# Kernel tuning notes

Hardware: AMD Instinct MI355X
Metric: run time of the kernel (lower is better)

Reference implementation:

```python
import jax, jax.numpy as jnp
import numpy as np

H = 256; NH = 8; DH = H // NH; L = 2; B = 32; S = 512; FIN = 199; A = 4


def _ln(x, g, b):
    m = jnp.mean(x, -1, keepdims=True)
    v = jnp.mean((x - m) ** 2, -1, keepdims=True)
    return (x - m) / jnp.sqrt(v + 1e-5) * g + b


def _grn(x, fc1w, fc1b, fc2w, fc2b, gw, gb, ggw, ggb, lg, lb):
    # GatedResidualNetwork, input_dim == output_dim so no skip layer, no context
    h = jax.nn.elu(x @ fc1w + fc1b)
    h = jax.nn.elu(h @ fc2w + fc2b)
    g = (h @ gw + gb) * jax.nn.sigmoid(h @ ggw + ggb)  # GLU
    return _ln(g + x, lg, lb)


def _attn(h, wq, bq, wk, bk, wv, bv, wo, bo):
    b, s, _ = h.shape
    q = (h @ wq + bq).reshape(b, s, NH, DH)
    k = (h @ wk + bk).reshape(b, s, NH, DH)
    v = (h @ wv + bv).reshape(b, s, NH, DH)
    scores = jnp.einsum('bqhd,bkhd->bhqk', q, k) / jnp.sqrt(jnp.float32(DH))
    mask = jnp.triu(jnp.ones((s, s), dtype=bool), 1)  # causal: mask strictly-future
    scores = jnp.where(mask, -jnp.inf, scores)
    aw = jax.nn.softmax(scores, axis=-1)
    ctx = jnp.einsum('bhqk,bkhd->bqhd', aw, v).reshape(b, s, H)
    return ctx @ wo + bo, aw


def _pe(s, d):
    pos = jnp.arange(s, dtype=jnp.float32)[:, None]
    div = jnp.exp(jnp.arange(0, d, 2, dtype=jnp.float32) * (-jnp.log(10000.0) / d))
    pe = jnp.zeros((s, d), dtype=jnp.float32)
    pe = pe.at[:, 0::2].set(jnp.sin(pos * div)).at[:, 1::2].set(jnp.cos(pos * div))
    return pe


def setup_inputs():
    key = jax.random.key(0)
    ks = iter(jax.random.split(key, 80))
    def nrm(shape, sc=0.02):
        return (jax.random.normal(next(ks), shape) * sc).astype(jnp.float32)
    d = {}
    d['x'] = jax.random.normal(next(ks), (B, S, FIN), dtype=jnp.float32)
    d['time_features'] = jax.random.normal(next(ks), (B, S, 3), dtype=jnp.float32)
    d['fp_w'] = nrm((FIN, H)); d['fp_b'] = jnp.zeros((H,), jnp.float32)
    d['tp_w'] = nrm((3, H));   d['tp_b'] = jnp.zeros((H,), jnp.float32)
    d['ip_w'] = nrm((H, H));   d['ip_b'] = jnp.zeros((H,), jnp.float32)
    for nm in ['wq', 'wk', 'wv', 'wo']:
        d[nm] = nrm((L, H, H))
    for nm in ['bq', 'bk', 'bv', 'bo']:
        d[nm] = jnp.zeros((L, H), jnp.float32)
    d['ln_g'] = jnp.ones((L, H), jnp.float32); d['ln_b'] = jnp.zeros((L, H), jnp.float32)
    for nm in ['g_fc1w', 'g_fc2w', 'g_gw', 'g_ggw']:
        d[nm] = nrm((L, H, H))
    for nm in ['g_fc1b', 'g_fc2b', 'g_gb', 'g_ggb']:
        d[nm] = jnp.zeros((L, H), jnp.float32)
    d['g_lg'] = jnp.ones((L, H), jnp.float32); d['g_lb'] = jnp.zeros((L, H), jnp.float32)
    for nm in ['f_fc1w', 'f_fc2w', 'f_gw', 'f_ggw']:
        d[nm] = nrm((H, H))
    for nm in ['f_fc1b', 'f_fc2b', 'f_gb', 'f_ggb']:
        d[nm] = jnp.zeros((H,), jnp.float32)
    d['f_lg'] = jnp.ones((H,), jnp.float32); d['f_lb'] = jnp.zeros((H,), jnp.float32)
    d['out_w'] = nrm((H, A)); d['out_b'] = jnp.zeros((A,), jnp.float32)
    return d


def reference(x, time_features, fp_w, fp_b, tp_w, tp_b, ip_w, ip_b,
              wq, bq, wk, bk, wv, bv, wo, bo, ln_g, ln_b,
              g_fc1w, g_fc1b, g_fc2w, g_fc2b, g_gw, g_gb, g_ggw, g_ggb, g_lg, g_lb,
              f_fc1w, f_fc1b, f_fc2w, f_fc2b, f_gw, f_gb, f_ggw, f_ggb, f_lg, f_lb,
              out_w, out_b):
    s = x.shape[1]
    hidden = (x @ fp_w + fp_b) + (time_features @ tp_w + tp_b)
    hidden = hidden @ ip_w + ip_b
    hidden = hidden + _pe(s, H)[None]
    aw = None
    for i in range(L):
        ao, aw = _attn(hidden, wq[i], bq[i], wk[i], bk[i], wv[i], bv[i], wo[i], bo[i])
        hidden = _ln(hidden + ao, ln_g[i], ln_b[i])
        hidden = _grn(hidden, g_fc1w[i], g_fc1b[i], g_fc2w[i], g_fc2b[i],
                      g_gw[i], g_gb[i], g_ggw[i], g_ggb[i], g_lg[i], g_lb[i])
    hidden = _grn(hidden, f_fc1w, f_fc1b, f_fc2w, f_fc2b, f_gw, f_gb, f_ggw, f_ggb, f_lg, f_lb)
    final = hidden[:, -1, :]
    logits = final @ out_w + out_b  # [B, A], one column per target asset
    return (logits, aw)
```

## Files before the change

### kernel.cpp

```cpp
#include <hip/hip_runtime.h>
#include <hip/hip_fp16.h>
#include <math.h>
#include <cstddef>

#define H 256
#define NH 8
#define DH 32
#define LAYERS 2
#define BB 32
#define SS 512
#define FINDIM 199
#define AA 4
#define T_TOK (BB*SS)
#define KIN 224
#define TPB 64

typedef unsigned short u16;
typedef unsigned int u32;
typedef __attribute__((ext_vector_type(8))) short short8;
typedef __attribute__((ext_vector_type(4))) float f4;

__device__ __forceinline__ float b2f(u16 v){
  unsigned u = ((unsigned)v) << 16;
  return __builtin_bit_cast(float, u);
}
__device__ __forceinline__ u16 f2b(float f){
  unsigned u = __builtin_bit_cast(unsigned, f);
  unsigned r = (u + 0x7fffu + ((u >> 16) & 1u)) >> 16;
  return (u16)r;
}
__device__ __forceinline__ float wave_sum(float v){
  #pragma unroll
  for (int mk=1; mk<64; mk<<=1) v += __shfl_xor(v, mk, 64);
  return v;
}

#define GLD_LDS16(g, l) \
  __builtin_amdgcn_global_load_lds((const __attribute__((address_space(1))) void*)(g), \
                                   (__attribute__((address_space(3))) void*)(l), 16, 0, 0)

#define SA (KIN+8)
#define SY (H+8)

template<int KC, int WK>
__device__ __forceinline__ void stage_acc64(
    const u16* Xl, int sx, const u16* __restrict__ Wt,
    int r0, int c0, int l16, int lq, f4 acc[2][4])
{
  #pragma unroll
  for (int mi=0;mi<2;mi++)
    #pragma unroll
    for (int ni=0;ni<4;ni++) acc[mi][ni] = (f4){0.f,0.f,0.f,0.f};
  #pragma unroll
  for (int kc=0;kc<KC;kc++){
    short8 af[2], bf[4];
    #pragma unroll
    for (int mi=0;mi<2;mi++)
      af[mi] = *(const short8*)&Xl[(r0 + mi*16 + l16)*sx + kc*32 + lq*8];
    #pragma unroll
    for (int ni=0;ni<4;ni++)
      bf[ni] = *(const short8*)(Wt + (size_t)(c0 + ni*16 + l16)*WK + kc*32 + lq*8);
    #pragma unroll
    for (int mi=0;mi<2;mi++)
      #pragma unroll
      for (int ni=0;ni<4;ni++)
        acc[mi][ni] = __builtin_amdgcn_mfma_f32_16x16x32_bf16(af[mi], bf[ni], acc[mi][ni], 0,0,0);
  }
}

template<int DO_ELU>
__device__ __forceinline__ void stage_store64(
    f4 acc[2][4], const float* __restrict__ bias,
    int r0, int c0, int l16, int lq, u16* Yl, int sy)
{
  #pragma unroll
  for (int ni=0;ni<4;ni++){
    int col = c0 + ni*16 + l16;
    float bc = bias[col];
    #pragma unroll
    for (int mi=0;mi<2;mi++){
      #pragma unroll
      for (int r=0;r<4;r++){
        int row = r0 + mi*16 + lq*4 + r;
        float v = acc[mi][ni][r] + bc;
        if (DO_ELU) v = v > 0.f ? v : expm1f(v);
        Yl[row*sy + col] = f2b(v);
      }
    }
  }
}

__device__ __forceinline__ void tile_load64(const u16* g, u16* Yl, int sy, int t){
  #pragma unroll
  for (int j=0;j<4;j++){
    int u = t + j*512;
    int row = u >> 5, cu = u & 31;
    *(short8*)&Yl[row*sy + cu*8] = *(const short8*)(g + (size_t)row*H + cu*8);
  }
}

template<int WB>
__device__ __forceinline__ void tile_ln64(
    u16* Yl, int sy, const float* __restrict__ g, const float* __restrict__ b,
    u16* out, int t)
{
  int w = t >> 6, lane = t & 63;
  #pragma unroll
  for (int rr=0;rr<8;rr++){
    int row = w*8 + rr;
    float xv[4];
    #pragma unroll
    for (int j=0;j<4;j++) xv[j] = b2f(Yl[row*sy + lane*4 + j]);
    float s=0.f, ss=0.f;
    #pragma unroll
    for (int j=0;j<4;j++){ s += xv[j]; ss += xv[j]*xv[j]; }
    s = wave_sum(s); ss = wave_sum(ss);
    float mean = s * (1.0f/H);
    float var  = ss * (1.0f/H) - mean*mean;
    float rstd = rsqrtf(var + 1e-5f);
    ushort4 o;
    int col = lane*4;
    o.x = f2b((xv[0]-mean)*rstd*g[col+0] + b[col+0]);
    o.y = f2b((xv[1]-mean)*rstd*g[col+1] + b[col+1]);
    o.z = f2b((xv[2]-mean)*rstd*g[col+2] + b[col+2]);
    o.w = f2b((xv[3]-mean)*rstd*g[col+3] + b[col+3]);
    *(ushort4*)(out + (size_t)row*H + col) = o;
    if (WB && row == 63) *(ushort4*)(Yl + row*sy + col) = o;
  }
}

struct WPtrs { const float* p[21]; };

__global__ __launch_bounds__(256) void wconv_kernel(WPtrs wp, u16* __restrict__ dst){
  __shared__ float tl[64][65];
  int mb = blockIdx.x >> 4, tile = blockIdx.x & 15;
  int k0 = (tile >> 2) * 64, n0 = (tile & 3) * 64;
  const float* src = wp.p[mb];
  int t = threadIdx.x;
  int r = t >> 4, cg = t & 15;
  #pragma unroll
  for (int p4=0;p4<4;p4++){
    f4 v = *(const f4*)(src + (size_t)(k0 + r + p4*16)*H + n0 + cg*4);
    tl[r+p4*16][cg*4+0]=v[0]; tl[r+p4*16][cg*4+1]=v[1];
    tl[r+p4*16][cg*4+2]=v[2]; tl[r+p4*16][cg*4+3]=v[3];
  }
  __syncthreads();
  u16* db = dst + (size_t)mb*H*H;
  #pragma unroll
  for (int p4=0;p4<4;p4++){
    int rn = r + p4*16;
    ushort4 o;
    o.x = f2b(tl[cg*4+0][rn]); o.y = f2b(tl[cg*4+1][rn]);
    o.z = f2b(tl[cg*4+2][rn]); o.w = f2b(tl[cg*4+3][rn]);
    *(ushort4*)(db + (size_t)(n0+rn)*H + k0 + cg*4) = o;
  }
}

__global__ __launch_bounds__(256) void wcat_kernel(
    const float* __restrict__ fp_w, const float* __restrict__ tp_w,
    u16* __restrict__ wcat){
  int idx = blockIdx.x*256 + threadIdx.x;
  if (idx >= 256*KIN) return;
  int n = idx / KIN, k2 = idx % KIN;
  float v = 0.f;
  if (k2 < FINDIM) v = fp_w[(size_t)k2*H + n];
  else if (k2 < FINDIM+3) v = tp_w[(size_t)(k2-FINDIM)*H + n];
  wcat[idx] = f2b(v);
}

__global__ __launch_bounds__(256) void xconv_kernel(
    const float* __restrict__ x, const float* __restrict__ tf,
    u16* __restrict__ ab){
  size_t idx = (size_t)blockIdx.x*256 + threadIdx.x;
  if (idx >= (size_t)T_TOK*KIN) return;
  int tok = idx / KIN, k2 = idx % KIN;
  float v = 0.f;
  if (k2 < FINDIM) v = x[(size_t)tok*FINDIM + k2];
  else if (k2 < FINDIM+3) v = tf[(size_t)tok*3 + (k2-FINDIM)];
  ab[idx] = f2b(v);
}

__global__ __launch_bounds__(512,2) void input_kernel(
    const u16* __restrict__ ab, const u16* __restrict__ wcat,
    const float* __restrict__ fp_b, const float* __restrict__ tp_b,
    const u16* __restrict__ ipw, const float* __restrict__ ip_b,
    u16* __restrict__ hid){
  __shared__ u16 Al[TPB*SA];
  __shared__ u16 Tl[TPB*SY];
  int t = threadIdx.x;
  int tok0 = blockIdx.x * TPB;
  int lane = t & 63, w = t >> 6;
  int l16 = lane & 15, lq = lane >> 4;
  int r0 = (w >> 2) * 32;
  int c0 = (w & 3) * 64;

  #pragma unroll
  for (int j=0;j<4;j++){
    int u = t + j*512;
    if (u < 1792){
      int row = u / 28, cu = u % 28;
      *(short8*)&Al[row*SA + cu*8] = *(const short8*)(ab + (size_t)(tok0+row)*KIN + cu*8);
    }
  }
  __syncthreads();

  f4 acc[2][4];
  stage_acc64<7, KIN>(Al, SA, wcat, r0, c0, l16, lq, acc);
  #pragma unroll
  for (int ni=0;ni<4;ni++){
    int col = c0 + ni*16 + l16;
    float bc = fp_b[col] + tp_b[col];
    #pragma unroll
    for (int mi=0;mi<2;mi++)
      #pragma unroll
      for (int r=0;r<4;r++){
        int row = r0 + mi*16 + lq*4 + r;
        Tl[row*SY + col] = f2b(acc[mi][ni][r] + bc);
      }
  }
  __syncthreads();

  stage_acc64<8, H>(Tl, SY, ipw, r0, c0, l16, lq, acc);
  #pragma unroll
  for (int ni=0;ni<4;ni++){
    int col = c0 + ni*16 + l16;
    float bc = ip_b[col];
    int ii = col >> 1;
    float div = __expf((float)(2*ii) * -0.03597789207803197f);
    #pragma unroll
    for (int mi=0;mi<2;mi++)
      #pragma unroll
      for (int r=0;r<4;r++){
        int row = r0 + mi*16 + lq*4 + r;
        int s = (tok0 + row) & (SS-1);
        float arg = (float)s * div;
        float pe = (col & 1) ? cosf(arg) : sinf(arg);
        hid[(size_t)(tok0+row)*H + col] = f2b(acc[mi][ni][r] + bc + pe);
      }
  }
}

__global__ __launch_bounds__(512,2) void oproj_ln_kernel(
    const u16* __restrict__ ctx, u16* __restrict__ hid,
    const u16* __restrict__ wo, const float* __restrict__ bo,
    const float* __restrict__ g, const float* __restrict__ b){
  __shared__ u16 Xl[TPB*SY];
  __shared__ u16 Rl[TPB*SY];
  int t = threadIdx.x;
  int tok0 = blockIdx.x * TPB;
  int lane = t & 63, w = t >> 6;
  int l16 = lane & 15, lq = lane >> 4;
  int r0 = (w >> 2) * 32;
  int c0 = (w & 3) * 64;
  u16* hb = hid + (size_t)tok0*H;

  tile_load64(ctx + (size_t)tok0*H, Xl, SY, t);
  tile_load64(hb, Rl, SY, t);
  __syncthreads();

  f4 acc[2][4];
  stage_acc64<8, H>(Xl, SY, wo, r0, c0, l16, lq, acc);
  __syncthreads();
  #pragma unroll
  for (int ni=0;ni<4;ni++){
    int col = c0 + ni*16 + l16;
    float bc = bo[col];
    #pragma unroll
    for (int mi=0;mi<2;mi++)
      #pragma unroll
      for (int r=0;r<4;r++){
        int row = r0 + mi*16 + lq*4 + r;
        float y = acc[mi][ni][r] + bc + b2f(Rl[row*SY + col]);
        Xl[row*SY + col] = f2b(y);
      }
  }
  __syncthreads();
  tile_ln64<0>(Xl, SY, g, b, hb, t);
}

template<int LOGITS>
__global__ __launch_bounds__(512,2) void grn_kernel(
    u16* __restrict__ hid,
    const u16* __restrict__ fc1, const u16* __restrict__ fc2,
    const u16* __restrict__ gw,  const u16* __restrict__ ggw,
    const float* __restrict__ b1, const float* __restrict__ b2,
    const float* __restrict__ gb, const float* __restrict__ ggb,
    const float* __restrict__ lg, const float* __restrict__ lb,
    const float* __restrict__ ow, const float* __restrict__ ob,
    float* __restrict__ lout){
  __shared__ u16 Xa[TPB*SY];
  __shared__ u16 Xb[TPB*SY];
  int t = threadIdx.x;
  int tok0 = blockIdx.x * TPB;
  int lane = t & 63, w = t >> 6;
  int l16 = lane & 15, lq = lane >> 4;
  int r0 = (w >> 2) * 32;
  int c0 = (w & 3) * 64;
  u16* hb = hid + (size_t)tok0*H;

  tile_load64(hb, Xa, SY, t);
  __syncthreads();

  f4 acc[2][4];
  stage_acc64<8, H>(Xa, SY, fc1, r0, c0, l16, lq, acc);
  stage_store64<1>(acc, b1, r0, c0, l16, lq, Xb, SY);
  __syncthreads();
  stage_acc64<8, H>(Xb, SY, fc2, r0, c0, l16, lq, acc);
  __syncthreads();
  stage_store64<1>(acc, b2, r0, c0, l16, lq, Xb, SY);
  __syncthreads();

  stage_acc64<8, H>(Xb, SY, ggw, r0, c0, l16, lq, acc);
  u32 sgp[2][4][2];
  #pragma unroll
  for (int mi=0;mi<2;mi++)
    #pragma unroll
    for (int ni=0;ni<4;ni++){
      float bc = ggb[c0 + ni*16 + l16];
      float s0 = 1.0f/(1.0f + __expf(-(acc[mi][ni][0]+bc)));
      float s1 = 1.0f/(1.0f + __expf(-(acc[mi][ni][1]+bc)));
      float s2 = 1.0f/(1.0f + __expf(-(acc[mi][ni][2]+bc)));
      float s3 = 1.0f/(1.0f + __expf(-(acc[mi][ni][3]+bc)));
      sgp[mi][ni][0] = __builtin_bit_cast(u32, __floats2half2_rn(s0, s1));
      sgp[mi][ni][1] = __builtin_bit_cast(u32, __floats2half2_rn(s2, s3));
    }

  stage_acc64<8, H>(Xb, SY, gw, r0, c0, l16, lq, acc);
  __syncthreads();
  #pragma unroll
  for (int ni=0;ni<4;ni++){
    int col = c0 + ni*16 + l16;
    float bc = gb[col];
    #pragma unroll
    for (int mi=0;mi<2;mi++){
      float2 s01 = __half22float2(__builtin_bit_cast(__half2, sgp[mi][ni][0]));
      float2 s23 = __half22float2(__builtin_bit_cast(__half2, sgp[mi][ni][1]));
      float sv[4] = {s01.x, s01.y, s23.x, s23.y};
      #pragma unroll
      for (int r=0;r<4;r++){
        int row = r0 + mi*16 + lq*4 + r;
        float y = (acc[mi][ni][r] + bc) * sv[r] + b2f(Xa[row*SY + col]);
        Xb[row*SY + col] = f2b(y);
      }
    }
  }
  __syncthreads();
  tile_ln64<LOGITS>(Xb, SY, lg, lb, hb, t);

  if (LOGITS){
    if ((tok0 & (SS-1)) == SS - TPB){
      __syncthreads();
      if (t < 64){
        int bidx = tok0 >> 9;
        float a0=0.f, a1=0.f, a2=0.f, a3=0.f;
        #pragma unroll
        for (int j=0;j<4;j++){
          int k = t*4 + j;
          float xv = b2f(Xb[63*SY + k]);
          f4 wr = *(const f4*)(ow + (size_t)k*AA);
          a0 = fmaf(xv, wr[0], a0);
          a1 = fmaf(xv, wr[1], a1);
          a2 = fmaf(xv, wr[2], a2);
          a3 = fmaf(xv, wr[3], a3);
        }
        a0 = wave_sum(a0); a1 = wave_sum(a1);
        a2 = wave_sum(a2); a3 = wave_sum(a3);
        if (t == 0){
          lout[bidx*AA+0] = a0 + ob[0];
          lout[bidx*AA+1] = a1 + ob[1];
          lout[bidx*AA+2] = a2 + ob[2];
          lout[bidx*AA+3] = a3 + ob[3];
        }
      }
    }
  }
}

struct GemmJob  { const u16* Wt; const float* bias; u16* C; };
struct GemmBatch{ GemmJob j[3]; };

__global__ __launch_bounds__(256) void gemm_bf16(
    const u16* __restrict__ A, GemmBatch jb) {
  __shared__ u16 smem[128*64 + 64*64];
  u16* As  = smem;
  u16* Wsm = smem + 128*64;
  const GemmJob job = jb.j[blockIdx.z];
  const u16* Wt = job.Wt;
  int t = threadIdx.x;
  int m0 = blockIdx.x * 128;
  int n0 = blockIdx.y * 64;
  int lane = t & 63, w = t >> 6;
  int wr = (w >> 1) * 64;
  int wc = (w & 1) * 32;
  int l16 = lane & 15, lq = lane >> 4;

  f4 acc[4][2];
  #pragma unroll
  for (int mi=0;mi<4;mi++)
    #pragma unroll
    for (int ni=0;ni<2;ni++) acc[mi][ni] = (f4){0.f,0.f,0.f,0.f};

  for (int k0=0;k0<256;k0+=64){
    #pragma unroll
    for (int ja=0;ja<4;ja++){
      int ub = (w*4 + ja)*64;
      int u  = ub + lane;
      int m  = u >> 3, c = u & 7, kx = c ^ (m & 7);
      const u16* g = A + (size_t)(m0+m)*H + k0 + kx*8;
      GLD_LDS16(g, As + (size_t)ub*8);
    }
    #pragma unroll
    for (int jb2=0;jb2<2;jb2++){
      int ub = (w*2 + jb2)*64;
      int u  = ub + lane;
      int n  = u >> 3, c = u & 7, kx = c ^ (n & 7);
      const u16* g = Wt + (size_t)(n0+n)*H + k0 + kx*8;
      GLD_LDS16(g, Wsm + (size_t)ub*8);
    }
    __syncthreads();
    #pragma unroll
    for (int kc=0;kc<2;kc++){
      short8 af[4], bf[2];
      int kx = kc*4 + lq;
      #pragma unroll
      for (int mi=0;mi<4;mi++){
        int m = wr + mi*16 + l16;
        int un = (m<<3) | (kx ^ (m&7));
        af[mi] = *(short8*)&As[un*8];
      }
      #pragma unroll
      for (int ni=0;ni<2;ni++){
        int n = wc + ni*16 + l16;
        int un = (n<<3) | (kx ^ (n&7));
        bf[ni] = *(short8*)&Wsm[un*8];
      }
      #pragma unroll
      for (int mi=0;mi<4;mi++)
        #pragma unroll
        for (int ni=0;ni<2;ni++)
          acc[mi][ni] = __builtin_amdgcn_mfma_f32_16x16x32_bf16(af[mi], bf[ni], acc[mi][ni], 0,0,0);
    }
    __syncthreads();
  }

  u16* Cl = smem;
  #pragma unroll
  for (int ni=0;ni<2;ni++){
    int coll = wc + ni*16 + l16;
    float bcol = job.bias[n0 + coll];
    #pragma unroll
    for (int mi=0;mi<4;mi++){
      #pragma unroll
      for (int r=0;r<4;r++){
        int rowl = wr + mi*16 + lq*4 + r;
        Cl[rowl*68 + coll] = f2b(acc[mi][ni][r] + bcol);
      }
    }
  }
  __syncthreads();
  #pragma unroll
  for (int q2=0;q2<4;q2++){
    int u = q2*256 + t;
    int row = u >> 3, cu = u & 7;
    short8 val = *(short8*)&Cl[row*68 + cu*8];
    *(short8*)(job.C + (size_t)(m0+row)*H + n0 + cu*8) = val;
  }
}

template<int WRITE_AW>
__global__ __launch_bounds__(512) void attn_kernel(
    const u16* __restrict__ q, const u16* __restrict__ k,
    const u16* __restrict__ v, float* __restrict__ aw,
    u16* __restrict__ ctx) {
  __shared__ u16 Vt[DH][SS+8];
  __shared__ u16 Plds[8][16][72];
  int t  = threadIdx.x;
  int zg = blockIdx.x;
  int bh = blockIdx.y;
  int b  = bh >> 3, h = bh & 7;
  int lane = t & 63, w = t >> 6;
  int l16 = lane & 15, lq = lane >> 4;
  const float scale = 0.17677669529663687f;

  int nrows = (zg+1)*128;
  for (int kk = t; kk < nrows; kk += 512){
    const u16* vp = v + ((size_t)(b*SS + kk))*H + h*DH;
    short8 r0v = *(const short8*)(vp);
    short8 r1v = *(const short8*)(vp+8);
    short8 r2v = *(const short8*)(vp+16);
    short8 r3v = *(const short8*)(vp+24);
    #pragma unroll
    for (int j=0;j<8;j++){
      Vt[j][kk]    = (u16)r0v[j];
      Vt[8+j][kk]  = (u16)r1v[j];
      Vt[16+j][kk] = (u16)r2v[j];
      Vt[24+j][kk] = (u16)r3v[j];
    }
  }
  __syncthreads();

  {
    int qt  = zg*2 + (w >> 2);
    int wq  = w & 3;
    int qr0 = qt*64 + wq*16;
    int KT  = qt*4 + wq + 1;
    short8 af = *(const short8*)(q + ((size_t)(b*SS + qr0 + l16))*H + h*DH + lq*8);

    float l[4] = {0.f,0.f,0.f,0.f};
    f4 o[2] = {(f4){0.f,0.f,0.f,0.f}, (f4){0.f,0.f,0.f,0.f}};

    #pragma unroll
    for (int c8=0;c8<8;c8++){
      if (c8*4 < KT){
        #pragma unroll
        for (int j=0;j<4;j++){
          int kt = c8*4 + j;
          float p[4] = {0.f,0.f,0.f,0.f};
          if (kt < KT){
            short8 bfr = *(const short8*)(k + ((size_t)(b*SS + kt*16 + l16))*H + h*DH + lq*8);
            f4 cc = (f4){0.f,0.f,0.f,0.f};
            cc = __builtin_amdgcn_mfma_f32_16x16x32_bf16(af, bfr, cc, 0,0,0);
            int col = kt*16 + l16;
            #pragma unroll
            for (int i=0;i<4;i++){
              int qi = qr0 + lq*4 + i;
              float sc = (col <= qi) ? cc[i]*scale : -3.0e38f;
              p[i] = __expf(sc);
              l[i] += p[i];
            }
          }
          #pragma unroll
          for (int i=0;i<4;i++) Plds[w][lq*4+i][j*16+l16] = f2b(p[i]);
        }
        #pragma unroll
        for (int kc=0;kc<2;kc++){
          short8 pa = *(short8*)&Plds[w][l16][kc*32 + lq*8];
          #pragma unroll
          for (int dt=0;dt<2;dt++){
            short8 vb = *(const short8*)&Vt[dt*16 + l16][c8*64 + kc*32 + lq*8];
            o[dt] = __builtin_amdgcn_mfma_f32_16x16x32_bf16(pa, vb, o[dt], 0,0,0);
          }
        }
      }
    }

    #pragma unroll
    for (int i=0;i<4;i++){
      #pragma unroll
      for (int mk=1; mk<16; mk<<=1) l[i] += __shfl_xor(l[i], mk, 64);
    }
    float inv[4];
    #pragma unroll
    for (int i=0;i<4;i++) inv[i] = 1.0f / l[i];

    if (WRITE_AW){
      float* ab = aw + (size_t)bh*SS*SS;
      for (int kt=0; kt<KT; kt++){
        short8 bfr = *(const short8*)(k + ((size_t)(b*SS + kt*16 + l16))*H + h*DH + lq*8);
        f4 cc = (f4){0.f,0.f,0.f,0.f};
        cc = __builtin_amdgcn_mfma_f32_16x16x32_bf16(af, bfr, cc, 0,0,0);
        int col = kt*16 + l16;
        #pragma unroll
        for (int i=0;i<4;i++){
          int qi = qr0 + lq*4 + i;
          float val = (col <= qi) ? __expf(cc[i]*scale)*inv[i] : 0.f;
          __builtin_nontemporal_store(val, &ab[(size_t)qi*SS + col]);
        }
      }
      int c4base = KT*4;
      f4 z = (f4){0.f,0.f,0.f,0.f};
      #pragma unroll
      for (int ri=0;ri<4;ri++){
        int row = qr0 + ri*4 + lq;
        for (int j=l16; j < 128 - c4base; j += 16)
          __builtin_nontemporal_store(z, (f4*)&ab[(size_t)row*SS + (size_t)(c4base+j)*4]);
      }
    }

    #pragma unroll
    for (int dt=0;dt<2;dt++){
      #pragma unroll
      for (int i=0;i<4;i++){
        int row = qr0 + lq*4 + i;
        ctx[((size_t)(b*SS + row))*H + h*DH + dt*16 + l16] = f2b(o[dt][i]*inv[i]);
      }
    }
  }
}

extern "C" void kernel_launch(void* const* d_in, const int* in_sizes, int n_in,
                              void* d_out, int out_size, void* d_ws, size_t ws_size,
                              hipStream_t stream){
  (void)in_sizes; (void)n_in; (void)out_size; (void)ws_size;
  const float* x      = (const float*)d_in[0];
  const float* tf     = (const float*)d_in[1];
  const float* fp_w   = (const float*)d_in[2];
  const float* fp_b   = (const float*)d_in[3];
  const float* tp_w   = (const float*)d_in[4];
  const float* tp_b   = (const float*)d_in[5];
  const float* ip_w   = (const float*)d_in[6];
  const float* ip_b   = (const float*)d_in[7];
  const float* wq     = (const float*)d_in[8];
  const float* wk     = (const float*)d_in[9];
  const float* wv     = (const float*)d_in[10];
  const float* wo     = (const float*)d_in[11];
  const float* bq     = (const float*)d_in[12];
  const float* bk     = (const float*)d_in[13];
  const float* bv     = (const float*)d_in[14];
  const float* bo     = (const float*)d_in[15];
  const float* ln_g   = (const float*)d_in[16];
  const float* ln_b   = (const float*)d_in[17];
  const float* g_fc1w = (const float*)d_in[18];
  const float* g_fc2w = (const float*)d_in[19];
  const float* g_gw   = (const float*)d_in[20];
  const float* g_ggw  = (const float*)d_in[21];
  const float* g_fc1b = (const float*)d_in[22];
  const float* g_fc2b = (const float*)d_in[23];
  const float* g_gb   = (const float*)d_in[24];
  const float* g_ggb  = (const float*)d_in[25];
  const float* g_lg   = (const float*)d_in[26];
  const float* g_lb   = (const float*)d_in[27];
  const float* f_fc1w = (const float*)d_in[28];
  const float* f_fc2w = (const float*)d_in[29];
  const float* f_gw   = (const float*)d_in[30];
  const float* f_ggw  = (const float*)d_in[31];
  const float* f_fc1b = (const float*)d_in[32];
  const float* f_fc2b = (const float*)d_in[33];
  const float* f_gb   = (const float*)d_in[34];
  const float* f_ggb  = (const float*)d_in[35];
  const float* f_lg   = (const float*)d_in[36];
  const float* f_lb   = (const float*)d_in[37];
  const float* out_w  = (const float*)d_in[38];
  const float* out_b  = (const float*)d_in[39];

  float* logits = (float*)d_out;
  float* aw     = logits + BB*AA;

  u16* wts = (u16*)d_ws;
  const size_t WMAT = (size_t)H*H;
  u16* wcat = wts  + 21*WMAT;
  u16* abuf = wcat + (size_t)H*KIN;
  u16* hid  = abuf + (size_t)T_TOK*KIN;
  size_t BUF = (size_t)T_TOK * H;
  u16* buf1 = hid  + BUF;
  u16* buf2 = buf1 + BUF;
  u16* buf3 = buf2 + BUF;

  WPtrs wp;
  wp.p[0]  = ip_w;
  wp.p[1]  = wq;        wp.p[2]  = wq + WMAT;
  wp.p[3]  = wk;        wp.p[4]  = wk + WMAT;
  wp.p[5]  = wv;        wp.p[6]  = wv + WMAT;
  wp.p[7]  = wo;        wp.p[8]  = wo + WMAT;
  wp.p[9]  = g_fc1w;    wp.p[10] = g_fc1w + WMAT;
  wp.p[11] = g_fc2w;    wp.p[12] = g_fc2w + WMAT;
  wp.p[13] = g_gw;      wp.p[14] = g_gw + WMAT;
  wp.p[15] = g_ggw;     wp.p[16] = g_ggw + WMAT;
  wp.p[17] = f_fc1w;    wp.p[18] = f_fc2w;
  wp.p[19] = f_gw;      wp.p[20] = f_ggw;
  const int WT_IP=0, WT_Q=1, WT_K=3, WT_V=5, WT_O=7,
            WT_FC1=9, WT_FC2=11, WT_GW=13, WT_GGW=15,
            WT_FFC1=17, WT_FFC2=18, WT_FGW=19, WT_FGGW=20;

  dim3 b256(256), b512(512);
  dim3 gAttn(4, BB*NH);
  dim3 gTok(T_TOK/TPB);

  wconv_kernel<<<21*16, b256, 0, stream>>>(wp, wts);
  wcat_kernel<<<(H*KIN+255)/256, b256, 0, stream>>>(fp_w, tp_w, wcat);
  xconv_kernel<<<(T_TOK*KIN+255)/256, b256, 0, stream>>>(x, tf, abuf);
  input_kernel<<<gTok, b512, 0, stream>>>(abuf, wcat, fp_b, tp_b,
                                          wts + (size_t)WT_IP*WMAT, ip_b, hid);

  for (int i=0;i<LAYERS;i++){
    const size_t BOFF = (size_t)i*H;
    GemmBatch gb;
    gb.j[0] = { wts + (size_t)(WT_Q+i)*WMAT, bq+BOFF, buf1 };
    gb.j[1] = { wts + (size_t)(WT_K+i)*WMAT, bk+BOFF, buf2 };
    gb.j[2] = { wts + (size_t)(WT_V+i)*WMAT, bv+BOFF, buf3 };
    gemm_bf16<<<dim3(T_TOK/128, H/64, 3), b256, 0, stream>>>(hid, gb);
    if (i == LAYERS-1)
      attn_kernel<1><<<gAttn, b512, 0, stream>>>(buf1, buf2, buf3, aw, buf1);
    else
      attn_kernel<0><<<gAttn, b512, 0, stream>>>(buf1, buf2, buf3, aw, buf1);
    oproj_ln_kernel<<<gTok, b512, 0, stream>>>(buf1, hid,
        wts + (size_t)(WT_O+i)*WMAT, bo+BOFF, ln_g+BOFF, ln_b+BOFF);
    grn_kernel<0><<<gTok, b512, 0, stream>>>(hid,
        wts + (size_t)(WT_FC1+i)*WMAT, wts + (size_t)(WT_FC2+i)*WMAT,
        wts + (size_t)(WT_GW+i)*WMAT,  wts + (size_t)(WT_GGW+i)*WMAT,
        g_fc1b+BOFF, g_fc2b+BOFF, g_gb+BOFF, g_ggb+BOFF,
        g_lg+BOFF, g_lb+BOFF, nullptr, nullptr, nullptr);
  }

  grn_kernel<1><<<gTok, b512, 0, stream>>>(hid,
      wts + (size_t)WT_FFC1*WMAT, wts + (size_t)WT_FFC2*WMAT,
      wts + (size_t)WT_FGW*WMAT,  wts + (size_t)WT_FGGW*WMAT,
      f_fc1b, f_fc2b, f_gb, f_ggb, f_lg, f_lb,
      out_w, out_b, logits);
}
```

Measured before the change: 666.0 us.

## Move attention-weight writeout into output-projection kernel as extra blocks

The last layer's attention kernel no longer writes the full causal attention-weight matrix. It stores only the per-row softmax reciprocal sums. Extra blocks appended to the output-projection/LayerNorm launch recompute QK^T and write the normalized weights, plus the zero fill, so this bandwidth-heavy store runs alongside the projection work instead of serializing the attention kernel. Attention output now goes to a separate buffer so Q stays intact for the recompute. The cost is a second QK^T pass and extra workspace.

```diff
diff --git a/kernel.cpp b/kernel.cpp
--- a/kernel.cpp
+++ b/kernel.cpp
@@ -240,16 +240,59 @@
   }
 }
 
+template<int AW>
 __global__ __launch_bounds__(512,2) void oproj_ln_kernel(
     const u16* __restrict__ ctx, u16* __restrict__ hid,
     const u16* __restrict__ wo, const float* __restrict__ bo,
-    const float* __restrict__ g, const float* __restrict__ b){
+    const float* __restrict__ g, const float* __restrict__ b,
+    const u16* __restrict__ q, const u16* __restrict__ k,
+    const float* __restrict__ linv, float* __restrict__ aw){
   __shared__ u16 Xl[TPB*SY];
   __shared__ u16 Rl[TPB*SY];
+  int bid = blockIdx.x;
   int t = threadIdx.x;
-  int tok0 = blockIdx.x * TPB;
   int lane = t & 63, w = t >> 6;
   int l16 = lane & 15, lq = lane >> 4;
+
+  if (AW && bid >= T_TOK/TPB){
+    int bh = bid - T_TOK/TPB;
+    int b2 = bh >> 3, h = bh & 7;
+    const float scale = 0.17677669529663687f;
+    float* ab = aw + (size_t)bh*SS*SS;
+    int qt = w;
+    #pragma unroll
+    for (int s=0;s<4;s++){
+      int qr0 = qt*64 + s*16;
+      int KT  = qt*4 + s + 1;
+      short8 af = *(const short8*)(q + ((size_t)(b2*SS + qr0 + l16))*H + h*DH + lq*8);
+      float iv[4];
+      #pragma unroll
+      for (int i=0;i<4;i++) iv[i] = linv[(size_t)bh*SS + qr0 + lq*4 + i];
+      for (int kt=0; kt<KT; kt++){
+        short8 bfr = *(const short8*)(k + ((size_t)(b2*SS + kt*16 + l16))*H + h*DH + lq*8);
+        f4 cc = (f4){0.f,0.f,0.f,0.f};
+        cc = __builtin_amdgcn_mfma_f32_16x16x32_bf16(af, bfr, cc, 0,0,0);
+        int col = kt*16 + l16;
+        #pragma unroll
+        for (int i=0;i<4;i++){
+          int qi = qr0 + lq*4 + i;
+          float val = (col <= qi) ? __expf(cc[i]*scale)*iv[i] : 0.f;
+          __builtin_nontemporal_store(val, &ab[(size_t)qi*SS + col]);
+        }
+      }
+      int c4base = KT*4;
+      f4 z = (f4){0.f,0.f,0.f,0.f};
+      #pragma unroll
+      for (int ri=0;ri<4;ri++){
+        int row = qr0 + ri*4 + lq;
+        for (int j=l16; j < 128 - c4base; j += 16)
+          __builtin_nontemporal_store(z, (f4*)&ab[(size_t)row*SS + (size_t)(c4base+j)*4]);
+      }
+    }
+    return;
+  }
+
+  int tok0 = bid * TPB;
   int r0 = (w >> 2) * 32;
   int c0 = (w & 3) * 64;
   u16* hb = hid + (size_t)tok0*H;
@@ -467,10 +510,10 @@
   }
 }
 
-template<int WRITE_AW>
+template<int SAVE_L>
 __global__ __launch_bounds__(512) void attn_kernel(
     const u16* __restrict__ q, const u16* __restrict__ k,
-    const u16* __restrict__ v, float* __restrict__ aw,
+    const u16* __restrict__ v, float* __restrict__ linv,
     u16* __restrict__ ctx) {
   __shared__ u16 Vt[DH][SS+8];
   __shared__ u16 Plds[8][16][72];
@@ -553,27 +596,11 @@
     #pragma unroll
     for (int i=0;i<4;i++) inv[i] = 1.0f / l[i];
 
-    if (WRITE_AW){
-      float* ab = aw + (size_t)bh*SS*SS;
-      for (int kt=0; kt<KT; kt++){
-        short8 bfr = *(const short8*)(k + ((size_t)(b*SS + kt*16 + l16))*H + h*DH + lq*8);
-        f4 cc = (f4){0.f,0.f,0.f,0.f};
-        cc = __builtin_amdgcn_mfma_f32_16x16x32_bf16(af, bfr, cc, 0,0,0);
-        int col = kt*16 + l16;
+    if (SAVE_L){
+      if (l16 == 0){
         #pragma unroll
-        for (int i=0;i<4;i++){
-          int qi = qr0 + lq*4 + i;
-          float val = (col <= qi) ? __expf(cc[i]*scale)*inv[i] : 0.f;
-          __builtin_nontemporal_store(val, &ab[(size_t)qi*SS + col]);
-        }
-      }
-      int c4base = KT*4;
-      f4 z = (f4){0.f,0.f,0.f,0.f};
-      #pragma unroll
-      for (int ri=0;ri<4;ri++){
-        int row = qr0 + ri*4 + lq;
-        for (int j=l16; j < 128 - c4base; j += 16)
-          __builtin_nontemporal_store(z, (f4*)&ab[(size_t)row*SS + (size_t)(c4base+j)*4]);
+        for (int i=0;i<4;i++)
+          linv[(size_t)bh*SS + qr0 + lq*4 + i] = inv[i];
       }
     }
 
@@ -645,6 +672,8 @@
   u16* buf1 = hid  + BUF;
   u16* buf2 = buf1 + BUF;
   u16* buf3 = buf2 + BUF;
+  u16* buf4 = buf3 + BUF;
+  float* linv = (float*)(buf4 + BUF);
 
   WPtrs wp;
   wp.p[0]  = ip_w;
@@ -679,12 +708,17 @@
     gb.j[1] = { wts + (size_t)(WT_K+i)*WMAT, bk+BOFF, buf2 };
     gb.j[2] = { wts + (size_t)(WT_V+i)*WMAT, bv+BOFF, buf3 };
     gemm_bf16<<<dim3(T_TOK/128, H/64, 3), b256, 0, stream>>>(hid, gb);
-    if (i == LAYERS-1)
-      attn_kernel<1><<<gAttn, b512, 0, stream>>>(buf1, buf2, buf3, aw, buf1);
-    else
-      attn_kernel<0><<<gAttn, b512, 0, stream>>>(buf1, buf2, buf3, aw, buf1);
-    oproj_ln_kernel<<<gTok, b512, 0, stream>>>(buf1, hid,
-        wts + (size_t)(WT_O+i)*WMAT, bo+BOFF, ln_g+BOFF, ln_b+BOFF);
+    if (i == LAYERS-1){
+      attn_kernel<1><<<gAttn, b512, 0, stream>>>(buf1, buf2, buf3, linv, buf4);
+      oproj_ln_kernel<1><<<dim3(T_TOK/TPB + BB*NH), b512, 0, stream>>>(
+          buf4, hid, wts + (size_t)(WT_O+i)*WMAT, bo+BOFF, ln_g+BOFF, ln_b+BOFF,
+          buf1, buf2, linv, aw);
+    } else {
+      attn_kernel<0><<<gAttn, b512, 0, stream>>>(buf1, buf2, buf3, linv, buf4);
+      oproj_ln_kernel<0><<<gTok, b512, 0, stream>>>(
+          buf4, hid, wts + (size_t)(WT_O+i)*WMAT, bo+BOFF, ln_g+BOFF, ln_b+BOFF,
+          nullptr, nullptr, nullptr, nullptr);
+    }
     grn_kernel<0><<<gTok, b512, 0, stream>>>(hid,
         wts + (size_t)(WT_FC1+i)*WMAT, wts + (size_t)(WT_FC2+i)*WMAT,
         wts + (size_t)(WT_GW+i)*WMAT,  wts + (size_t)(WT_GGW+i)*WMAT,
```

Result: slower. 690.4 us (+3.7%).

## Split attention key range across two wave groups per query tile

Applied to the files above, without the earlier changes.

Each block now handles one 64-row query tile instead of two, and the grid doubles in x. The two groups of four waves each take half of the key chunks for the same query rows, then merge partial row sums and outputs through LDS before normalising. The aw write is split the same way. This is meant to balance the causal work and raise parallelism, at the cost of extra syncs, an LDS reduction, and reloading V per block.

```diff
diff --git a/kernel.cpp b/kernel.cpp
--- a/kernel.cpp
+++ b/kernel.cpp
@@ -475,14 +475,14 @@
   __shared__ u16 Vt[DH][SS+8];
   __shared__ u16 Plds[8][16][72];
   int t  = threadIdx.x;
-  int zg = blockIdx.x;
+  int qt = blockIdx.x;
   int bh = blockIdx.y;
   int b  = bh >> 3, h = bh & 7;
   int lane = t & 63, w = t >> 6;
   int l16 = lane & 15, lq = lane >> 4;
   const float scale = 0.17677669529663687f;
 
-  int nrows = (zg+1)*128;
+  int nrows = (qt+1)*64;
   for (int kk = t; kk < nrows; kk += 512){
     const u16* vp = v + ((size_t)(b*SS + kk))*H + h*DH;
     short8 r0v = *(const short8*)(vp);
@@ -499,63 +499,24 @@
   }
   __syncthreads();
 
-  {
-    int qt  = zg*2 + (w >> 2);
-    int wq  = w & 3;
-    int qr0 = qt*64 + wq*16;
-    int KT  = qt*4 + wq + 1;
-    short8 af = *(const short8*)(q + ((size_t)(b*SS + qr0 + l16))*H + h*DH + lq*8);
-
-    float l[4] = {0.f,0.f,0.f,0.f};
-    f4 o[2] = {(f4){0.f,0.f,0.f,0.f}, (f4){0.f,0.f,0.f,0.f}};
-
-    #pragma unroll
-    for (int c8=0;c8<8;c8++){
-      if (c8*4 < KT){
-        #pragma unroll
-        for (int j=0;j<4;j++){
-          int kt = c8*4 + j;
-          float p[4] = {0.f,0.f,0.f,0.f};
-          if (kt < KT){
-            short8 bfr = *(const short8*)(k + ((size_t)(b*SS + kt*16 + l16))*H + h*DH + lq*8);
-            f4 cc = (f4){0.f,0.f,0.f,0.f};
-            cc = __builtin_amdgcn_mfma_f32_16x16x32_bf16(af, bfr, cc, 0,0,0);
-            int col = kt*16 + l16;
-            #pragma unroll
-            for (int i=0;i<4;i++){
-              int qi = qr0 + lq*4 + i;
-              float sc = (col <= qi) ? cc[i]*scale : -3.0e38f;
-              p[i] = __expf(sc);
-              l[i] += p[i];
-            }
-          }
-          #pragma unroll
-          for (int i=0;i<4;i++) Plds[w][lq*4+i][j*16+l16] = f2b(p[i]);
-        }
-        #pragma unroll
-        for (int kc=0;kc<2;kc++){
-          short8 pa = *(short8*)&Plds[w][l16][kc*32 + lq*8];
-          #pragma unroll
-          for (int dt=0;dt<2;dt++){
-            short8 vb = *(const short8*)&Vt[dt*16 + l16][c8*64 + kc*32 + lq*8];
-            o[dt] = __builtin_amdgcn_mfma_f32_16x16x32_bf16(pa, vb, o[dt], 0,0,0);
-          }
-        }
-      }
-    }
-
-    #pragma unroll
-    for (int i=0;i<4;i++){
-      #pragma unroll
-      for (int mk=1; mk<16; mk<<=1) l[i] += __shfl_xor(l[i], mk, 64);
-    }
-    float inv[4];
-    #pragma unroll
-    for (int i=0;i<4;i++) inv[i] = 1.0f / l[i];
-
-    if (WRITE_AW){
-      float* ab = aw + (size_t)bh*SS*SS;
-      for (int kt=0; kt<KT; kt++){
+  int s   = w & 3;
+  int qr0 = qt*64 + s*16;
+  int KT  = qt*4 + s + 1;
+  int G   = (KT + 3) >> 2;
+  int gh  = (G + 1) >> 1;
+  int g0  = (w < 4) ? 0  : gh;
+  int g1  = (w < 4) ? gh : G;
+  short8 af = *(const short8*)(q + ((size_t)(b*SS + qr0 + l16))*H + h*DH + lq*8);
+
+  float l[4] = {0.f,0.f,0.f,0.f};
+  f4 o[2] = {(f4){0.f,0.f,0.f,0.f}, (f4){0.f,0.f,0.f,0.f}};
+
+  for (int c8 = g0; c8 < g1; c8++){
+    #pragma unroll
+    for (int j=0;j<4;j++){
+      int kt = c8*4 + j;
+      float p[4] = {0.f,0.f,0.f,0.f};
+      if (kt < KT){
         short8 bfr = *(const short8*)(k + ((size_t)(b*SS + kt*16 + l16))*H + h*DH + lq*8);
         f4 cc = (f4){0.f,0.f,0.f,0.f};
         cc = __builtin_amdgcn_mfma_f32_16x16x32_bf16(af, bfr, cc, 0,0,0);
@@ -563,10 +524,89 @@
         #pragma unroll
         for (int i=0;i<4;i++){
           int qi = qr0 + lq*4 + i;
-          float val = (col <= qi) ? __expf(cc[i]*scale)*inv[i] : 0.f;
-          __builtin_nontemporal_store(val, &ab[(size_t)qi*SS + col]);
+          float sc = (col <= qi) ? cc[i]*scale : -3.0e38f;
+          p[i] = __expf(sc);
+          l[i] += p[i];
         }
       }
+      #pragma unroll
+      for (int i=0;i<4;i++) Plds[w][lq*4+i][j*16+l16] = f2b(p[i]);
+    }
+    #pragma unroll
+    for (int kc=0;kc<2;kc++){
+      short8 pa = *(short8*)&Plds[w][l16][kc*32 + lq*8];
+      #pragma unroll
+      for (int dt=0;dt<2;dt++){
+        short8 vb = *(const short8*)&Vt[dt*16 + l16][c8*64 + kc*32 + lq*8];
+        o[dt] = __builtin_amdgcn_mfma_f32_16x16x32_bf16(pa, vb, o[dt], 0,0,0);
+      }
+    }
+  }
+
+  float* Pf = (float*)&Plds[0][0][0];
+  __syncthreads();
+  if (w >= 4){
+    float* dst = Pf + ((size_t)s*64 + lane)*13;
+    #pragma unroll
+    for (int i=0;i<4;i++) dst[i]   = l[i];
+    #pragma unroll
+    for (int i=0;i<4;i++) dst[4+i] = o[0][i];
+    #pragma unroll
+    for (int i=0;i<4;i++) dst[8+i] = o[1][i];
+  }
+  __syncthreads();
+  float inv[4];
+  if (w < 4){
+    float* src = Pf + ((size_t)s*64 + lane)*13;
+    #pragma unroll
+    for (int i=0;i<4;i++) l[i]    += src[i];
+    #pragma unroll
+    for (int i=0;i<4;i++) o[0][i] += src[4+i];
+    #pragma unroll
+    for (int i=0;i<4;i++) o[1][i] += src[8+i];
+    #pragma unroll
+    for (int i=0;i<4;i++){
+      #pragma unroll
+      for (int mk=1; mk<16; mk<<=1) l[i] += __shfl_xor(l[i], mk, 64);
+      inv[i] = 1.0f / l[i];
+    }
+    #pragma unroll
+    for (int dt=0;dt<2;dt++){
+      #pragma unroll
+      for (int i=0;i<4;i++){
+        int row = qr0 + lq*4 + i;
+        ctx[((size_t)(b*SS + row))*H + h*DH + dt*16 + l16] = f2b(o[dt][i]*inv[i]);
+      }
+    }
+    if (WRITE_AW){
+      #pragma unroll
+      for (int i=0;i<4;i++) src[i] = inv[i];
+    }
+  }
+
+  if (WRITE_AW){
+    __syncthreads();
+    if (w >= 4){
+      const float* src = Pf + ((size_t)s*64 + lane)*13;
+      #pragma unroll
+      for (int i=0;i<4;i++) inv[i] = src[i];
+    }
+    float* ab = aw + (size_t)bh*SS*SS;
+    int k_lo = g0*4;
+    int k_hi = (g1*4 < KT) ? g1*4 : KT;
+    for (int kt = k_lo; kt < k_hi; kt++){
+      short8 bfr = *(const short8*)(k + ((size_t)(b*SS + kt*16 + l16))*H + h*DH + lq*8);
+      f4 cc = (f4){0.f,0.f,0.f,0.f};
+      cc = __builtin_amdgcn_mfma_f32_16x16x32_bf16(af, bfr, cc, 0,0,0);
+      int col = kt*16 + l16;
+      #pragma unroll
+      for (int i=0;i<4;i++){
+        int qi = qr0 + lq*4 + i;
+        float val = (col <= qi) ? __expf(cc[i]*scale)*inv[i] : 0.f;
+        __builtin_nontemporal_store(val, &ab[(size_t)qi*SS + col]);
+      }
+    }
+    if (w >= 4){
       int c4base = KT*4;
       f4 z = (f4){0.f,0.f,0.f,0.f};
       #pragma unroll
@@ -574,15 +614,6 @@
         int row = qr0 + ri*4 + lq;
         for (int j=l16; j < 128 - c4base; j += 16)
           __builtin_nontemporal_store(z, (f4*)&ab[(size_t)row*SS + (size_t)(c4base+j)*4]);
-      }
-    }
-
-    #pragma unroll
-    for (int dt=0;dt<2;dt++){
-      #pragma unroll
-      for (int i=0;i<4;i++){
-        int row = qr0 + lq*4 + i;
-        ctx[((size_t)(b*SS + row))*H + h*DH + dt*16 + l16] = f2b(o[dt][i]*inv[i]);
       }
     }
   }
@@ -663,7 +694,7 @@
             WT_FFC1=17, WT_FFC2=18, WT_FGW=19, WT_FGGW=20;
 
   dim3 b256(256), b512(512);
-  dim3 gAttn(4, BB*NH);
+  dim3 gAttn(8, BB*NH);
   dim3 gTok(T_TOK/TPB);
 
   wconv_kernel<<<21*16, b256, 0, stream>>>(wp, wts);
```

Result: no change. 663.2 us (-0.4%).

## Compute transposed scores in attention to keep P in registers, dropping LDS round-trip

Applied to the files above, without the earlier changes.

The attention kernel now computes S^T (K as the A operand, Q as B), so each lane already holds the probabilities in the layout the P·V MFMA wants. P goes straight into packed bf16 operand registers via v_cvt_pk_bf16_f32 instead of being written to a per-wave LDS tile and read back. The V operand is rebuilt from two 32-bit pairs to match the permuted k ordering. This removes LDS stores, reads and the implicit wave sync per chunk, at the cost of scattered 4-byte V loads from LDS and an extra shuffle to redistribute the row normalizers. The ctx store is also moved ahead of the attention-weight writes.

```diff
diff --git a/kernel.cpp b/kernel.cpp
--- a/kernel.cpp
+++ b/kernel.cpp
@@ -19,6 +19,7 @@
 typedef unsigned int u32;
 typedef __attribute__((ext_vector_type(8))) short short8;
 typedef __attribute__((ext_vector_type(4))) float f4;
+typedef __attribute__((ext_vector_type(4))) unsigned int u32x4;
 
 __device__ __forceinline__ float b2f(u16 v){
   unsigned u = ((unsigned)v) << 16;
@@ -28,6 +29,11 @@
   unsigned u = __builtin_bit_cast(unsigned, f);
   unsigned r = (u + 0x7fffu + ((u >> 16) & 1u)) >> 16;
   return (u16)r;
+}
+__device__ __forceinline__ u32 cvt_pk_bf16(float lo, float hi){
+  u32 r;
+  asm volatile("v_cvt_pk_bf16_f32 %0, %1, %2" : "=v"(r) : "v"(lo), "v"(hi));
+  return r;
 }
 __device__ __forceinline__ float wave_sum(float v){
   #pragma unroll
@@ -473,7 +479,6 @@
     const u16* __restrict__ v, float* __restrict__ aw,
     u16* __restrict__ ctx) {
   __shared__ u16 Vt[DH][SS+8];
-  __shared__ u16 Plds[8][16][72];
   int t  = threadIdx.x;
   int zg = blockIdx.x;
   int bh = blockIdx.y;
@@ -506,52 +511,62 @@
     int KT  = qt*4 + wq + 1;
     short8 af = *(const short8*)(q + ((size_t)(b*SS + qr0 + l16))*H + h*DH + lq*8);
 
-    float l[4] = {0.f,0.f,0.f,0.f};
+    float lsum = 0.f;
     f4 o[2] = {(f4){0.f,0.f,0.f,0.f}, (f4){0.f,0.f,0.f,0.f}};
 
-    #pragma unroll
-    for (int c8=0;c8<8;c8++){
-      if (c8*4 < KT){
-        #pragma unroll
-        for (int j=0;j<4;j++){
-          int kt = c8*4 + j;
-          float p[4] = {0.f,0.f,0.f,0.f};
-          if (kt < KT){
-            short8 bfr = *(const short8*)(k + ((size_t)(b*SS + kt*16 + l16))*H + h*DH + lq*8);
-            f4 cc = (f4){0.f,0.f,0.f,0.f};
-            cc = __builtin_amdgcn_mfma_f32_16x16x32_bf16(af, bfr, cc, 0,0,0);
-            int col = kt*16 + l16;
-            #pragma unroll
-            for (int i=0;i<4;i++){
-              int qi = qr0 + lq*4 + i;
-              float sc = (col <= qi) ? cc[i]*scale : -3.0e38f;
-              p[i] = __expf(sc);
-              l[i] += p[i];
-            }
-          }
+    for (int c8=0; c8*4 < KT; c8++){
+      u32 pk[4][2];
+      #pragma unroll
+      for (int j=0;j<4;j++){
+        int kt = c8*4 + j;
+        float p[4] = {0.f,0.f,0.f,0.f};
+        if (kt < KT){
+          short8 bfr = *(const short8*)(k + ((size_t)(b*SS + kt*16 + l16))*H + h*DH + lq*8);
+          f4 cc = (f4){0.f,0.f,0.f,0.f};
+          cc = __builtin_amdgcn_mfma_f32_16x16x32_bf16(bfr, af, cc, 0,0,0);
           #pragma unroll
-          for (int i=0;i<4;i++) Plds[w][lq*4+i][j*16+l16] = f2b(p[i]);
-        }
-        #pragma unroll
-        for (int kc=0;kc<2;kc++){
-          short8 pa = *(short8*)&Plds[w][l16][kc*32 + lq*8];
-          #pragma unroll
-          for (int dt=0;dt<2;dt++){
-            short8 vb = *(const short8*)&Vt[dt*16 + l16][c8*64 + kc*32 + lq*8];
-            o[dt] = __builtin_amdgcn_mfma_f32_16x16x32_bf16(pa, vb, o[dt], 0,0,0);
+          for (int i=0;i<4;i++){
+            int kk2 = kt*16 + lq*4 + i;
+            float sc = (kk2 <= qr0 + l16) ? cc[i]*scale : -3.0e38f;
+            p[i] = __expf(sc);
+            lsum += p[i];
           }
         }
-      }
-    }
-
-    #pragma unroll
-    for (int i=0;i<4;i++){
-      #pragma unroll
-      for (int mk=1; mk<16; mk<<=1) l[i] += __shfl_xor(l[i], mk, 64);
-    }
-    float inv[4];
-    #pragma unroll
-    for (int i=0;i<4;i++) inv[i] = 1.0f / l[i];
+        pk[j][0] = cvt_pk_bf16(p[0], p[1]);
+        pk[j][1] = cvt_pk_bf16(p[2], p[3]);
+      }
+      #pragma unroll
+      for (int kc=0;kc<2;kc++){
+        int kt0 = c8*4 + 2*kc, kt1 = kt0 + 1;
+        short8 pa = __builtin_bit_cast(short8,
+            (u32x4){pk[2*kc][0], pk[2*kc][1], pk[2*kc+1][0], pk[2*kc+1][1]});
+        #pragma unroll
+        for (int dt=0;dt<2;dt++){
+          const u32* vrow = (const u32*)&Vt[dt*16 + l16][0];
+          int i0 = kt0*8 + lq*2;
+          int i1 = kt1*8 + lq*2;
+          short8 vb = __builtin_bit_cast(short8,
+              (u32x4){vrow[i0], vrow[i0+1], vrow[i1], vrow[i1+1]});
+          o[dt] = __builtin_amdgcn_mfma_f32_16x16x32_bf16(pa, vb, o[dt], 0,0,0);
+        }
+      }
+    }
+
+    lsum += __shfl_xor(lsum, 16, 64);
+    lsum += __shfl_xor(lsum, 32, 64);
+    float invq = 1.0f / lsum;
+    float inv4[4];
+    #pragma unroll
+    for (int i=0;i<4;i++) inv4[i] = __shfl(invq, lq*4 + i, 64);
+
+    #pragma unroll
+    for (int dt=0;dt<2;dt++){
+      #pragma unroll
+      for (int i=0;i<4;i++){
+        int row = qr0 + lq*4 + i;
+        ctx[((size_t)(b*SS + row))*H + h*DH + dt*16 + l16] = f2b(o[dt][i]*inv4[i]);
+      }
+    }
 
     if (WRITE_AW){
       float* ab = aw + (size_t)bh*SS*SS;
@@ -563,7 +578,7 @@
         #pragma unroll
         for (int i=0;i<4;i++){
           int qi = qr0 + lq*4 + i;
-          float val = (col <= qi) ? __expf(cc[i]*scale)*inv[i] : 0.f;
+          float val = (col <= qi) ? __expf(cc[i]*scale)*inv4[i] : 0.f;
           __builtin_nontemporal_store(val, &ab[(size_t)qi*SS + col]);
         }
       }
@@ -574,15 +589,6 @@
         int row = qr0 + ri*4 + lq;
         for (int j=l16; j < 128 - c4base; j += 16)
           __builtin_nontemporal_store(z, (f4*)&ab[(size_t)row*SS + (size_t)(c4base+j)*4]);
-      }
-    }
-
-    #pragma unroll
-    for (int dt=0;dt<2;dt++){
-      #pragma unroll
-      for (int i=0;i<4;i++){
-        int row = qr0 + lq*4 + i;
-        ctx[((size_t)(b*SS + row))*H + h*DH + dt*16 + l16] = f2b(o[dt][i]*inv[i]);
       }
     }
   }
```

After: 663.4 us. About the same (-0.4%).
